# Performance work log

Hardware: AMD Instinct MI355X
Metric: run time of the kernel (lower is better)

Reference implementation:

```python
import jax, jax.numpy as jnp
import numpy as np
import math


def setup_inputs() -> dict:
    key = jax.random.key(0)
    k1, k2, k3, k4 = jax.random.split(key, 4)
    B, H, N, DK = 4, 8, 512, 64
    return {
        "query": jax.random.normal(k1, (B * H, N, DK), dtype=jnp.float32),
        "key": jax.random.normal(k2, (B * H, N, DK), dtype=jnp.float32),
        "value": jax.random.normal(k3, (B * H, N, DK), dtype=jnp.float32),
        "relation": jax.random.normal(k4, (B, N, N, DK), dtype=jnp.float32),
        "mask": jnp.zeros((B, H, N, N), dtype=jnp.float32),
        "head_num": H,
    }


def reference(query, key, value, relation, mask, head_num):
    # query/key/value: (B*H, N, dk); relation: (B, N, N, dk); mask: (B, H, N, N)
    BH, N, dk = query.shape
    B = BH // head_num
    scale = 1.0 / math.sqrt(dk)
    # content scores: (B*H, N, N)
    scores = jnp.einsum("bnd,bmd->bnm", query, key) * scale
    # relative scores: broadcast relation over heads instead of repeating it
    qh = query.reshape(B, head_num, N, dk)
    rel_scores = jnp.einsum("bhid,bijd->bhij", qh, relation)  # (B, H, N, N)
    scores = scores.reshape(B, head_num, N, N) + rel_scores + mask
    attn = jax.nn.softmax(scores, axis=-1)  # (B, H, N, N)
    attn_flat = attn.reshape(BH, N, N)
    # content values: (B*H, N, dk)
    self_att_val = jnp.einsum("bnm,bmd->bnd", attn_flat, value)
    # relation-weighted values: (B, H, N, dk)
    rel_att_val = jnp.einsum("bhij,bijd->bhid", attn, relation)
    return self_att_val + rel_att_val.reshape(BH, N, dk)
```

## Files before the change

kernel.cpp:

```cpp
#include <hip/hip_runtime.h>
#include <math.h>

#define NB  4
#define NH  8
#define SEQ 512
#define DKC 64
#define TJ  64
#define RSTR 68

__global__ __launch_bounds__(256) void relattn_fwd(
    const float* __restrict__ Q, const float* __restrict__ K,
    const float* __restrict__ V, const float* __restrict__ R,
    const float* __restrict__ M, float* __restrict__ O)
{
    __shared__ __align__(16) float Rs[TJ][RSTR];
    __shared__ __align__(16) float Ps[NH][TJ];

    const int bid = blockIdx.x;
    const int b   = bid >> 9;
    const int i   = bid & (SEQ - 1);
    const int t   = threadIdx.x;
    const int h   = t >> 5;
    const int g   = t & 31;
    const int d4v = g & 15;
    const int jh  = g >> 4;

    const float scale = 0.125f;

    const float* qrow = Q + (size_t)((b*NH + h)*SEQ + i) * DKC;
    float4 qreg[16];
#pragma unroll
    for (int d4 = 0; d4 < 16; ++d4)
        qreg[d4] = reinterpret_cast<const float4*>(qrow)[d4];

    const float* kbase = K + (size_t)(b*NH + h) * SEQ * DKC;
    const float* vbase = V + (size_t)(b*NH + h) * SEQ * DKC;
    const float* rbase = R + (size_t)(b*SEQ + i) * SEQ * DKC;
    const float* mbase = M + (size_t)((b*NH + h)*SEQ + i) * SEQ;

    float m = -INFINITY, l = 0.f;
    float ax = 0.f, ay = 0.f, az = 0.f, aw = 0.f;

    for (int j0 = 0; j0 < SEQ; j0 += TJ) {
        __syncthreads();
        {
            const float4* g4 = reinterpret_cast<const float4*>(rbase + (size_t)j0 * DKC);
#pragma unroll
            for (int kk = 0; kk < 4; ++kk) {
                int idx4 = t + 256*kk;
                float4 val = g4[idx4];
                int jj = idx4 >> 4;
                int dd = (idx4 & 15) << 2;
                *reinterpret_cast<float4*>(&Rs[jj][dd]) = val;
            }
        }
        __syncthreads();

        const int jt0 = g, jt1 = g + 32;
        float s0 = 0.f, s1 = 0.f;
        const float4* ka4 = reinterpret_cast<const float4*>(kbase + (size_t)(j0 + jt0) * DKC);
        const float4* kb4 = reinterpret_cast<const float4*>(kbase + (size_t)(j0 + jt1) * DKC);
#pragma unroll
        for (int d4 = 0; d4 < 16; ++d4) {
            float4 qv = qreg[d4];
            float4 ra = *reinterpret_cast<const float4*>(&Rs[jt0][d4 << 2]);
            float4 rb = *reinterpret_cast<const float4*>(&Rs[jt1][d4 << 2]);
            float4 ka = ka4[d4];
            float4 kb = kb4[d4];
            s0 = fmaf(qv.x, fmaf(scale, ka.x, ra.x),
                 fmaf(qv.y, fmaf(scale, ka.y, ra.y),
                 fmaf(qv.z, fmaf(scale, ka.z, ra.z),
                 fmaf(qv.w, fmaf(scale, ka.w, ra.w), s0))));
            s1 = fmaf(qv.x, fmaf(scale, kb.x, rb.x),
                 fmaf(qv.y, fmaf(scale, kb.y, rb.y),
                 fmaf(qv.z, fmaf(scale, kb.z, rb.z),
                 fmaf(qv.w, fmaf(scale, kb.w, rb.w), s1))));
        }
        s0 += mbase[j0 + jt0];
        s1 += mbase[j0 + jt1];

        float tm = fmaxf(s0, s1);
#pragma unroll
        for (int off = 1; off < 32; off <<= 1) tm = fmaxf(tm, __shfl_xor(tm, off));
        float mn  = fmaxf(m, tm);
        float fac = __expf(m - mn);
        float p0  = __expf(s0 - mn);
        float p1  = __expf(s1 - mn);
        float ps  = p0 + p1;
#pragma unroll
        for (int off = 1; off < 32; off <<= 1) ps += __shfl_xor(ps, off);
        l = l * fac + ps;
        m = mn;
        Ps[h][jt0] = p0;
        Ps[h][jt1] = p1;
        ax *= fac; ay *= fac; az *= fac; aw *= fac;

        const int jbeg = jh << 5;
#pragma unroll
        for (int jj = 0; jj < 32; jj += 4) {
            int jt = jbeg + jj;
            float4 pv = *reinterpret_cast<const float4*>(&Ps[h][jt]);
#pragma unroll
            for (int u = 0; u < 4; ++u) {
                float p = (u == 0) ? pv.x : (u == 1) ? pv.y : (u == 2) ? pv.z : pv.w;
                float4 vv = *reinterpret_cast<const float4*>(
                                vbase + (size_t)(j0 + jt + u) * DKC + (d4v << 2));
                float4 rr = *reinterpret_cast<const float4*>(&Rs[jt + u][d4v << 2]);
                ax = fmaf(p, vv.x + rr.x, ax);
                ay = fmaf(p, vv.y + rr.y, ay);
                az = fmaf(p, vv.z + rr.z, az);
                aw = fmaf(p, vv.w + rr.w, aw);
            }
        }
    }

    ax += __shfl_xor(ax, 16);
    ay += __shfl_xor(ay, 16);
    az += __shfl_xor(az, 16);
    aw += __shfl_xor(aw, 16);
    const float inv = 1.0f / l;
    if (jh == 0) {
        float4 o = make_float4(ax * inv, ay * inv, az * inv, aw * inv);
        *reinterpret_cast<float4*>(O + (size_t)((b*NH + h)*SEQ + i) * DKC + (d4v << 2)) = o;
    }
}

extern "C" void kernel_launch(void* const* d_in, const int* in_sizes, int n_in,
                              void* d_out, int out_size, void* d_ws, size_t ws_size,
                              hipStream_t stream) {
    const float* Q = (const float*)d_in[0];
    const float* K = (const float*)d_in[1];
    const float* V = (const float*)d_in[2];
    const float* R = (const float*)d_in[3];
    const float* M = (const float*)d_in[4];
    float* O = (float*)d_out;
    relattn_fwd<<<dim3(NB * SEQ), dim3(256), 0, stream>>>(Q, K, V, R, M, O);
}
```

Measured before the change: 818.5 us.

## Double-buffer relation tiles through registers and split score dot products across lanes

```diff
diff --git a/kernel.cpp b/kernel.cpp
--- a/kernel.cpp
+++ b/kernel.cpp
@@ -13,7 +13,7 @@
     const float* __restrict__ V, const float* __restrict__ R,
     const float* __restrict__ M, float* __restrict__ O)
 {
-    __shared__ __align__(16) float Rs[TJ][RSTR];
+    __shared__ __align__(16) float Rs[2][TJ][RSTR];
     __shared__ __align__(16) float Ps[NH][TJ];
 
     const int bid = blockIdx.x;
@@ -22,90 +22,108 @@
     const int t   = threadIdx.x;
     const int h   = t >> 5;
     const int g   = t & 31;
+    const int dq  = g & 3;
+    const int jq  = g >> 2;
     const int d4v = g & 15;
     const int jh  = g >> 4;
 
     const float scale = 0.125f;
 
     const float* qrow = Q + (size_t)((b*NH + h)*SEQ + i) * DKC;
-    float4 qreg[16];
+    float4 qreg[4];
 #pragma unroll
-    for (int d4 = 0; d4 < 16; ++d4)
-        qreg[d4] = reinterpret_cast<const float4*>(qrow)[d4];
+    for (int u = 0; u < 4; ++u)
+        qreg[u] = reinterpret_cast<const float4*>(qrow)[dq*4 + u];
 
     const float* kbase = K + (size_t)(b*NH + h) * SEQ * DKC;
     const float* vbase = V + (size_t)(b*NH + h) * SEQ * DKC;
     const float* rbase = R + (size_t)(b*SEQ + i) * SEQ * DKC;
     const float* mbase = M + (size_t)((b*NH + h)*SEQ + i) * SEQ;
+    const float4* rg4  = reinterpret_cast<const float4*>(rbase);
+
+    float4 rstage[4];
+#pragma unroll
+    for (int kk = 0; kk < 4; ++kk) rstage[kk] = rg4[t + 256*kk];
 
     float m = -INFINITY, l = 0.f;
     float ax = 0.f, ay = 0.f, az = 0.f, aw = 0.f;
 
-    for (int j0 = 0; j0 < SEQ; j0 += TJ) {
-        __syncthreads();
-        {
-            const float4* g4 = reinterpret_cast<const float4*>(rbase + (size_t)j0 * DKC);
+    for (int t8 = 0; t8 < 8; ++t8) {
+        const int buf = t8 & 1;
+        const int j0  = t8 * TJ;
+
 #pragma unroll
-            for (int kk = 0; kk < 4; ++kk) {
-                int idx4 = t + 256*kk;
-                float4 val = g4[idx4];
-                int jj = idx4 >> 4;
-                int dd = (idx4 & 15) << 2;
-                *reinterpret_cast<float4*>(&Rs[jj][dd]) = val;
-            }
+        for (int kk = 0; kk < 4; ++kk) {
+            int idx4 = t + 256*kk;
+            *reinterpret_cast<float4*>(&Rs[buf][idx4 >> 4][(idx4 & 15) << 2]) = rstage[kk];
         }
         __syncthreads();
 
-        const int jt0 = g, jt1 = g + 32;
-        float s0 = 0.f, s1 = 0.f;
-        const float4* ka4 = reinterpret_cast<const float4*>(kbase + (size_t)(j0 + jt0) * DKC);
-        const float4* kb4 = reinterpret_cast<const float4*>(kbase + (size_t)(j0 + jt1) * DKC);
+        if (t8 < 7) {
+            const float4* gnext = rg4 + (size_t)(t8 + 1) * (TJ * DKC / 4);
 #pragma unroll
-        for (int d4 = 0; d4 < 16; ++d4) {
-            float4 qv = qreg[d4];
-            float4 ra = *reinterpret_cast<const float4*>(&Rs[jt0][d4 << 2]);
-            float4 rb = *reinterpret_cast<const float4*>(&Rs[jt1][d4 << 2]);
-            float4 ka = ka4[d4];
-            float4 kb = kb4[d4];
-            s0 = fmaf(qv.x, fmaf(scale, ka.x, ra.x),
-                 fmaf(qv.y, fmaf(scale, ka.y, ra.y),
-                 fmaf(qv.z, fmaf(scale, ka.z, ra.z),
-                 fmaf(qv.w, fmaf(scale, ka.w, ra.w), s0))));
-            s1 = fmaf(qv.x, fmaf(scale, kb.x, rb.x),
-                 fmaf(qv.y, fmaf(scale, kb.y, rb.y),
-                 fmaf(qv.z, fmaf(scale, kb.z, rb.z),
-                 fmaf(qv.w, fmaf(scale, kb.w, rb.w), s1))));
+            for (int kk = 0; kk < 4; ++kk) rstage[kk] = gnext[t + 256*kk];
         }
-        s0 += mbase[j0 + jt0];
-        s1 += mbase[j0 + jt1];
 
-        float tm = fmaxf(s0, s1);
+        float sreg[8];
 #pragma unroll
-        for (int off = 1; off < 32; off <<= 1) tm = fmaxf(tm, __shfl_xor(tm, off));
-        float mn  = fmaxf(m, tm);
-        float fac = __expf(m - mn);
-        float p0  = __expf(s0 - mn);
-        float p1  = __expf(s1 - mn);
-        float ps  = p0 + p1;
+        for (int p = 0; p < 8; ++p) {
+            const int j = p*8 + jq;
+            const float4* k4 = reinterpret_cast<const float4*>(
+                                   kbase + (size_t)(j0 + j) * DKC) + dq*4;
+            float acc = 0.f;
 #pragma unroll
-        for (int off = 1; off < 32; off <<= 1) ps += __shfl_xor(ps, off);
+            for (int u = 0; u < 4; ++u) {
+                float4 kv = k4[u];
+                float4 rv = *reinterpret_cast<const float4*>(&Rs[buf][j][dq*16 + u*4]);
+                float4 qv = qreg[u];
+                acc = fmaf(qv.x, fmaf(scale, kv.x, rv.x), acc);
+                acc = fmaf(qv.y, fmaf(scale, kv.y, rv.y), acc);
+                acc = fmaf(qv.z, fmaf(scale, kv.z, rv.z), acc);
+                acc = fmaf(qv.w, fmaf(scale, kv.w, rv.w), acc);
+            }
+            acc += __shfl_xor(acc, 1);
+            acc += __shfl_xor(acc, 2);
+            sreg[p] = acc + mbase[j0 + j];
+        }
+
+        float tm = sreg[0];
+#pragma unroll
+        for (int p = 1; p < 8; ++p) tm = fmaxf(tm, sreg[p]);
+        tm = fmaxf(tm, __shfl_xor(tm, 4));
+        tm = fmaxf(tm, __shfl_xor(tm, 8));
+        tm = fmaxf(tm, __shfl_xor(tm, 16));
+        const float mn  = fmaxf(m, tm);
+        const float fac = __expf(m - mn);
+        float ps = 0.f;
+#pragma unroll
+        for (int p = 0; p < 8; ++p) {
+            float pv = __expf(sreg[p] - mn);
+            sreg[p] = pv;
+            ps += pv;
+        }
+        ps += __shfl_xor(ps, 4);
+        ps += __shfl_xor(ps, 8);
+        ps += __shfl_xor(ps, 16);
         l = l * fac + ps;
         m = mn;
-        Ps[h][jt0] = p0;
-        Ps[h][jt1] = p1;
+        if (dq == 0) {
+#pragma unroll
+            for (int p = 0; p < 8; ++p) Ps[h][p*8 + jq] = sreg[p];
+        }
         ax *= fac; ay *= fac; az *= fac; aw *= fac;
 
         const int jbeg = jh << 5;
 #pragma unroll
         for (int jj = 0; jj < 32; jj += 4) {
-            int jt = jbeg + jj;
+            const int jt = jbeg + jj;
             float4 pv = *reinterpret_cast<const float4*>(&Ps[h][jt]);
 #pragma unroll
             for (int u = 0; u < 4; ++u) {
                 float p = (u == 0) ? pv.x : (u == 1) ? pv.y : (u == 2) ? pv.z : pv.w;
                 float4 vv = *reinterpret_cast<const float4*>(
                                 vbase + (size_t)(j0 + jt + u) * DKC + (d4v << 2));
-                float4 rr = *reinterpret_cast<const float4*>(&Rs[jt + u][d4v << 2]);
+                float4 rr = *reinterpret_cast<const float4*>(&Rs[buf][jt + u][d4v << 2]);
                 ax = fmaf(p, vv.x + rr.x, ax);
                 ay = fmaf(p, vv.y + rr.y, ay);
                 az = fmaf(p, vv.z + rr.z, az);
```

Measured after the change: 681.8 us. 1.2x faster.
